# Optimization experiments

Measured on AMD Instinct MI355X. Metric: run time of the kernel, lower is better.

The kernel has to match this reference:

```python
import jax, jax.numpy as jnp
import numpy as np

N_NODES = 1601   # fixed by in_adj Parameter shape in the source
EMB = 300        # EMB_SIZE
LAYERS = 3       # process_num
B, L = 2048, 64  # batch_size, label_num


def setup_inputs() -> dict:
    key = jax.random.key(0)
    k1, k2, k3, k4 = jax.random.split(key, 4)
    return {
        "label_set": jax.random.randint(k1, (B, L), 0, N_NODES),
        "in_adj": jax.random.uniform(k2, (N_NODES, N_NODES), dtype=jnp.float32),
        "embeddings": jax.random.normal(k3, (N_NODES, EMB), dtype=jnp.float32),
        "linear_w": jax.random.normal(k4, (LAYERS, EMB, EMB), dtype=jnp.float32) * 0.05,
    }


def _norm_matrix(m):
    # m: [B, L, L]; add self loops, symmetric D^-1/2 A D^-1/2 with D = column sums
    n = m.shape[1]
    m = m + jnp.eye(n, dtype=m.dtype)
    d = jnp.sum(m, axis=1) ** -0.5            # [B, L] (sum over axis=1, as in torch code)
    return m * d[:, None, :] * d[:, :, None]


def reference(label_set, in_adj, embeddings, linear_w):
    # Gather per-batch dense neighbor adjacency: neighbor[b,i,j] = in_adj[label[b,i], label[b,j]]
    neighbor = in_adj[label_set[:, :, None], label_set[:, None, :]]   # [B, L, L]
    adj = _norm_matrix(neighbor)
    h = embeddings[label_set]                                          # [B, L, EMB]
    for i in range(linear_w.shape[0]):
        # linear projection (Linear bias=False: x @ W^T) then adjacency aggregation
        h = jnp.einsum('bij,bje->bie', adj, h @ linear_w[i].T)
    return h
```

## Files before the change

kernel.cpp:

```cpp
#include <hip/hip_runtime.h>

#define NN   1601
#define EMB  300
#define NB   2048
#define L    64
#define TSTR 304
#define S    72

typedef __attribute__((ext_vector_type(8))) short bf16x8;
typedef __attribute__((ext_vector_type(4))) float f32x4;

static __device__ __forceinline__ ushort f2b(float x) {
  union { float f; unsigned u; } c; c.f = x;
  unsigned u = c.u;
  return (ushort)((u + 0x7FFFu + ((u >> 16) & 1u)) >> 16);
}
static __device__ __forceinline__ float b2f(ushort h) {
  union { unsigned u; float f; } c; c.u = ((unsigned)h) << 16; return c.f;
}

#define LD8(p, r, c) (*(const bf16x8*)&(p)[(size_t)(r) * S + (c)])
#define MFMA(a, bm, acc) __builtin_amdgcn_mfma_f32_16x16x32_bf16((a), (bm), (acc), 0, 0, 0)

template <int BT, int BF16OUT>
__device__ __forceinline__ void gemm_body(ushort* arena,
                                          const float* __restrict__ A,
                                          const float* __restrict__ B,
                                          void* __restrict__ Cout,
                                          int M, int AS, int BS, int KG,
                                          int mb, int nb) {
  ushort* Ahi = arena;
  ushort* Alo = arena + L * S;
  ushort* Bhi = arena + 2 * L * S;
  ushort* Blo = arena + 3 * L * S;
  int tid = threadIdx.x;
  int lane = tid & 63, w = tid >> 6;
  int lrow = lane & 15, lk = lane >> 4;

  f32x4 acc[4];
  #pragma unroll
  for (int t = 0; t < 4; ++t) acc[t] = (f32x4){0.f, 0.f, 0.f, 0.f};

  for (int kc = 0; kc < 5; ++kc) {
    int k0 = 64 * kc;
    for (int idx = tid; idx < 64 * 16; idx += 256) {
      int r = idx >> 4, c4 = (idx & 15) * 4;
      int m = mb * 64 + r, k = k0 + c4;
      float4 v = make_float4(0.f, 0.f, 0.f, 0.f);
      if (m < M && k < KG) v = *(const float4*)&A[(size_t)m * AS + k];
      ushort4 h4, l4;
      h4.x = f2b(v.x); l4.x = f2b(v.x - b2f(h4.x));
      h4.y = f2b(v.y); l4.y = f2b(v.y - b2f(h4.y));
      h4.z = f2b(v.z); l4.z = f2b(v.z - b2f(h4.z));
      h4.w = f2b(v.w); l4.w = f2b(v.w - b2f(h4.w));
      *(ushort4*)&Ahi[r * S + c4] = h4;
      *(ushort4*)&Alo[r * S + c4] = l4;
    }
    for (int idx = tid; idx < 64 * 16; idx += 256) {
      int r = idx >> 4, c4 = (idx & 15) * 4;
      if (BT) {
        int n = nb * 64 + r, k = k0 + c4;
        float4 v = make_float4(0.f, 0.f, 0.f, 0.f);
        if (n < 300 && k < 300) v = *(const float4*)&B[(size_t)n * BS + k];
        ushort4 h4, l4;
        h4.x = f2b(v.x); l4.x = f2b(v.x - b2f(h4.x));
        h4.y = f2b(v.y); l4.y = f2b(v.y - b2f(h4.y));
        h4.z = f2b(v.z); l4.z = f2b(v.z - b2f(h4.z));
        h4.w = f2b(v.w); l4.w = f2b(v.w - b2f(h4.w));
        *(ushort4*)&Bhi[r * S + c4] = h4;
        *(ushort4*)&Blo[r * S + c4] = l4;
      } else {
        int k = k0 + r, n = nb * 64 + c4;
        float4 v = make_float4(0.f, 0.f, 0.f, 0.f);
        if (k < 300 && n < 300) v = *(const float4*)&B[(size_t)k * BS + n];
        #pragma unroll
        for (int q = 0; q < 4; ++q) {
          float xq = (q == 0) ? v.x : (q == 1) ? v.y : (q == 2) ? v.z : v.w;
          ushort hi = f2b(xq);
          Bhi[(size_t)(c4 + q) * S + r] = hi;
          Blo[(size_t)(c4 + q) * S + r] = f2b(xq - b2f(hi));
        }
      }
    }
    __syncthreads();
    #pragma unroll
    for (int ks = 0; ks < 2; ++ks) {
      bf16x8 ah = LD8(Ahi, 16 * w + lrow, 32 * ks + 8 * lk);
      bf16x8 al = LD8(Alo, 16 * w + lrow, 32 * ks + 8 * lk);
      #pragma unroll
      for (int t = 0; t < 4; ++t) {
        bf16x8 bh = LD8(Bhi, 16 * t + lrow, 32 * ks + 8 * lk);
        bf16x8 bl = LD8(Blo, 16 * t + lrow, 32 * ks + 8 * lk);
        acc[t] = MFMA(ah, bh, acc[t]);
        acc[t] = MFMA(ah, bl, acc[t]);
        acc[t] = MFMA(al, bh, acc[t]);
      }
    }
    __syncthreads();
  }
  #pragma unroll
  for (int t = 0; t < 4; ++t) {
    int n = nb * 64 + 16 * t + lrow;
    int mbase = mb * 64 + 16 * w + 4 * lk;
    if (n < TSTR) {
      #pragma unroll
      for (int r = 0; r < 4; ++r) {
        int m = mbase + r;
        if (m < M) {
          if (BF16OUT) ((ushort*)Cout)[(size_t)m * TSTR + n] = f2b(acc[t][r]);
          else         ((float*)Cout)[(size_t)m * TSTR + n] = acc[t][r];
        }
      }
    }
  }
}

__global__ __launch_bounds__(256, 4) void k_pre1(const float* __restrict__ in_adj,
                                                 unsigned char* __restrict__ adj8,
                                                 const float* __restrict__ emb,
                                                 const float* __restrict__ lw,
                                                 float* __restrict__ E1,
                                                 float* __restrict__ T) {
  __shared__ __align__(16) ushort arena[4 * L * S];
  const float* W1 = lw;
  const float* W2 = lw + (size_t)EMB * EMB;
  const float* W3 = lw + 2 * (size_t)EMB * EMB;
  int bid = blockIdx.x;
  if (bid < 25) {
    gemm_body<0, 0>(arena, W3, W2, T, 300, 300, 300, 300, bid / 5, bid % 5);
  } else if (bid < 155) {
    int rid = bid - 25;
    gemm_body<1, 0>(arena, emb, W1, E1, NN, 300, 300, 300, rid % 26, rid / 26);
  } else {
    int b2 = bid - 155;
    const int total = NN * NN;
    const int n4 = total >> 2;
    int i = b2 * 256 + threadIdx.x;
    for (int i4 = i; i4 < n4; i4 += 1024 * 256) {
      float4 v = *(const float4*)&in_adj[4 * i4];
      uchar4 q;
      q.x = (unsigned char)__float2int_rn(v.x * 255.f);
      q.y = (unsigned char)__float2int_rn(v.y * 255.f);
      q.z = (unsigned char)__float2int_rn(v.z * 255.f);
      q.w = (unsigned char)__float2int_rn(v.w * 255.f);
      *(uchar4*)&adj8[4 * i4] = q;
    }
    if (i == 0)
      adj8[total - 1] = (unsigned char)__float2int_rn(in_adj[total - 1] * 255.f);
  }
}

__device__ __forceinline__ void a3_body(ushort* arena, int* lab, float (*ps)[L],
                                        float* dv, const int* __restrict__ labels,
                                        const unsigned char* __restrict__ adj8,
                                        ushort* __restrict__ a3g, int b) {
  ushort* buf0 = arena;
  ushort* buf1 = arena + L * S;
  ushort* buf2 = arena + 2 * L * S;
  ushort* buf3 = arena + 3 * L * S;
  int tid = threadIdx.x, j = tid & 63, g = tid >> 6;
  if (tid < L) lab[tid] = labels[(size_t)b * L + tid];
  __syncthreads();
  int labj = lab[j];

  float raw[16];
  float cs = 0.f;
  #pragma unroll
  for (int q = 0; q < 16; ++q) {
    int i = g + 4 * q;
    float v = (float)adj8[(size_t)lab[i] * NN + labj];
    v += (i == j) ? 255.f : 0.f;
    raw[q] = v; cs += v;
  }
  ps[g][j] = cs;
  __syncthreads();
  if (tid < L) dv[tid] = 1.f / sqrtf(ps[0][tid] + ps[1][tid] + ps[2][tid] + ps[3][tid]);
  __syncthreads();

  float dj = dv[j];
  #pragma unroll
  for (int q = 0; q < 16; ++q) {
    int i = g + 4 * q;
    float a = raw[q] * dv[i] * dj;
    ushort hi = f2b(a);
    ushort lo = f2b(a - b2f(hi));
    buf0[(size_t)i * S + j] = hi;
    buf1[(size_t)i * S + j] = lo;
    buf2[(size_t)j * S + i] = hi;
    buf3[(size_t)j * S + i] = lo;
  }
  __syncthreads();

  int lane = tid & 63, w = tid >> 6;
  int lrow = lane & 15, lk = lane >> 4;
  int m0 = 16 * w;

  bf16x8 ah0 = LD8(buf0, m0 + lrow, 8 * lk);
  bf16x8 ah1 = LD8(buf0, m0 + lrow, 32 + 8 * lk);
  bf16x8 al0 = LD8(buf1, m0 + lrow, 8 * lk);
  bf16x8 al1 = LD8(buf1, m0 + lrow, 32 + 8 * lk);

  {
    f32x4 acc[4];
    #pragma unroll
    for (int t = 0; t < 4; ++t) {
      f32x4 a = {0.f, 0.f, 0.f, 0.f};
      bf16x8 bh = LD8(buf2, 16 * t + lrow, 8 * lk);
      bf16x8 bl = LD8(buf3, 16 * t + lrow, 8 * lk);
      a = MFMA(ah0, bh, a); a = MFMA(ah0, bl, a); a = MFMA(al0, bh, a);
      bh = LD8(buf2, 16 * t + lrow, 32 + 8 * lk);
      bl = LD8(buf3, 16 * t + lrow, 32 + 8 * lk);
      a = MFMA(ah1, bh, a); a = MFMA(ah1, bl, a); a = MFMA(al1, bh, a);
      acc[t] = a;
    }
    __syncthreads();
    #pragma unroll
    for (int t = 0; t < 4; ++t) {
      ushort4 h4, l4;
      float x;
      x = acc[t][0]; h4.x = f2b(x); l4.x = f2b(x - b2f(h4.x));
      x = acc[t][1]; h4.y = f2b(x); l4.y = f2b(x - b2f(h4.y));
      x = acc[t][2]; h4.z = f2b(x); l4.z = f2b(x - b2f(h4.z));
      x = acc[t][3]; h4.w = f2b(x); l4.w = f2b(x - b2f(h4.w));
      *(ushort4*)&buf2[(size_t)(16 * t + lrow) * S + m0 + 4 * lk] = h4;
      *(ushort4*)&buf3[(size_t)(16 * t + lrow) * S + m0 + 4 * lk] = l4;
    }
  }
  __syncthreads();

  {
    f32x4 acc[4];
    #pragma unroll
    for (int t = 0; t < 4; ++t) {
      f32x4 a = {0.f, 0.f, 0.f, 0.f};
      bf16x8 bh = LD8(buf2, 16 * t + lrow, 8 * lk);
      bf16x8 bl = LD8(buf3, 16 * t + lrow, 8 * lk);
      a = MFMA(ah0, bh, a); a = MFMA(ah0, bl, a); a = MFMA(al0, bh, a);
      bh = LD8(buf2, 16 * t + lrow, 32 + 8 * lk);
      bl = LD8(buf3, 16 * t + lrow, 32 + 8 * lk);
      a = MFMA(ah1, bh, a); a = MFMA(ah1, bl, a); a = MFMA(al1, bh, a);
      acc[t] = a;
    }
    #pragma unroll
    for (int t = 0; t < 4; ++t)
      #pragma unroll
      for (int r = 0; r < 4; ++r)
        buf0[(size_t)(m0 + 4 * lk + r) * S + 16 * t + lrow] = f2b(acc[t][r]);
  }
  __syncthreads();

  int4* dst = (int4*)(a3g + (size_t)b * (L * L));
  #pragma unroll
  for (int q = 0; q < 2; ++q) {
    int id = tid + 256 * q;
    int r = id >> 3, c8 = (id & 7) << 3;
    dst[id] = *(const int4*)&buf0[(size_t)r * S + c8];
  }
}

__global__ __launch_bounds__(256, 4) void k_pre2(const int* __restrict__ labels,
                                                 const unsigned char* __restrict__ adj8,
                                                 ushort* __restrict__ a3g,
                                                 const float* __restrict__ E1,
                                                 const float* __restrict__ T,
                                                 ushort* __restrict__ t0bf) {
  __shared__ __align__(16) ushort arena[4 * L * S];
  __shared__ int   lab[L];
  __shared__ float ps[4][L];
  __shared__ float dv[L];
  int bid = blockIdx.x;
  if (bid < NB) {
    a3_body(arena, lab, ps, dv, labels, adj8, a3g, bid);
  } else {
    int rid = bid - NB;
    gemm_body<1, 1>(arena, E1, T, t0bf, NN, TSTR, TSTR, TSTR, rid % 26, rid / 26);
  }
}

__global__ __launch_bounds__(256, 6) void k_out(const int* __restrict__ labels,
                                                const ushort* __restrict__ a3g,
                                                const ushort* __restrict__ t0bf,
                                                float* __restrict__ out) {
  __shared__ __align__(16) ushort A3L[L * S];
  __shared__ __align__(16) ushort Tt[80 * S];
  int bid = blockIdx.x;
  int b = bid >> 2, c = bid & 3;
  int tid = threadIdx.x, j = tid & 63, g = tid >> 6;
  int labj = labels[(size_t)b * L + j];

  const int4* a3p = (const int4*)(a3g + (size_t)b * (L * L));
  #pragma unroll
  for (int q = 0; q < 2; ++q) {
    int id = tid + 256 * q;
    int r = id >> 3, c8 = (id & 7) << 3;
    *(int4*)&A3L[(size_t)r * S + c8] = a3p[id];
  }
  int base = 80 * c;
  int rows80 = (c == 3) ? 64 : 80;
  const ushort* trow = t0bf + (size_t)labj * TSTR + base;
  for (int e = 8 * g; e < rows80; e += 32) {
    union { int4 v; ushort u[8]; } uu;
    uu.v = *(const int4*)(trow + e);
    #pragma unroll
    for (int q = 0; q < 8; ++q) Tt[(size_t)(e + q) * S + j] = uu.u[q];
  }
  __syncthreads();

  int lane = tid & 63, w = tid >> 6;
  int lrow = lane & 15, lk = lane >> 4;
  int m0 = 16 * w;
  bf16x8 fb0 = LD8(A3L, m0 + lrow, 8 * lk);
  bf16x8 fb1 = LD8(A3L, m0 + lrow, 32 + 8 * lk);
  float* orow = out + ((size_t)b * L + m0 + lrow) * EMB;

  int nt = (c == 3) ? 4 : 5;
  for (int t = 0; t < nt; ++t) {
    bf16x8 a0 = LD8(Tt, 16 * t + lrow, 8 * lk);
    bf16x8 a1 = LD8(Tt, 16 * t + lrow, 32 + 8 * lk);
    f32x4 o = {0.f, 0.f, 0.f, 0.f};
    o = MFMA(a0, fb0, o);
    o = MFMA(a1, fb1, o);
    int e0 = base + 16 * t + 4 * lk;
    if (e0 < EMB) *(f32x4*)&orow[e0] = o;
  }
}

extern "C" void kernel_launch(void* const* d_in, const int* in_sizes, int n_in,
                              void* d_out, int out_size, void* d_ws, size_t ws_size,
                              hipStream_t stream) {
  (void)in_sizes; (void)n_in; (void)out_size; (void)ws_size;
  const int*   labels = (const int*)d_in[0];
  const float* in_adj = (const float*)d_in[1];
  const float* emb    = (const float*)d_in[2];
  const float* lw     = (const float*)d_in[3];
  float* out = (float*)d_out;

  char* base = (char*)d_ws;
  unsigned char* adj8 = (unsigned char*)base;
  float*  T    = (float*)(base + 2563216);
  float*  E1   = (float*)(base + 2928016);
  ushort* t0bf = (ushort*)(base + 4874832);
  ushort* a3g  = (ushort*)(base + 5848240);

  k_pre1<<<1179, 256, 0, stream>>>(in_adj, adj8, emb, lw, E1, T);
  k_pre2<<<2178, 256, 0, stream>>>(labels, adj8, a3g, E1, T, t0bf);
  k_out <<<4 * NB, 256, 0, stream>>>(labels, a3g, t0bf, out);
}
```

Before: 108.9 us.

## Halve k_pre2 LDS arena to raise occupancy and reorder gemm blocks first

The adjacency-cube body now reuses two LDS buffers instead of four. It rebuilds the transposed hi/lo split after the A fragments are loaded into registers, which halves the shared-memory arena and lets the launch bound request 8 blocks per CU. A dedicated gemm2 body handles the E1·T product with the smaller arena, and its 130 blocks are scheduled ahead of the 2048 per-batch blocks so the long GEMM tiles start early. k_out's launch bound is raised to 7 and its output stores become nontemporal. The cost is extra barriers and a second pass of bf16 conversion writes.

```diff
diff --git a/kernel.cpp b/kernel.cpp
--- a/kernel.cpp
+++ b/kernel.cpp
@@ -110,6 +110,85 @@
           if (BF16OUT) ((ushort*)Cout)[(size_t)m * TSTR + n] = f2b(acc[t][r]);
           else         ((float*)Cout)[(size_t)m * TSTR + n] = acc[t][r];
         }
+      }
+    }
+  }
+}
+
+__device__ __forceinline__ void gemm2_body(ushort* arena,
+                                           const float* __restrict__ A,
+                                           const float* __restrict__ B,
+                                           ushort* __restrict__ Cout,
+                                           int M, int mb, int nb) {
+  ushort* buf0 = arena;
+  ushort* buf1 = arena + L * S;
+  int tid = threadIdx.x;
+  int lane = tid & 63, w = tid >> 6;
+  int lrow = lane & 15, lk = lane >> 4;
+
+  f32x4 acc[4];
+  #pragma unroll
+  for (int t = 0; t < 4; ++t) acc[t] = (f32x4){0.f, 0.f, 0.f, 0.f};
+
+  for (int kc = 0; kc < 5; ++kc) {
+    int k0 = 64 * kc;
+    for (int idx = tid; idx < 64 * 16; idx += 256) {
+      int r = idx >> 4, c4 = (idx & 15) * 4;
+      int m = mb * 64 + r, k = k0 + c4;
+      float4 v = make_float4(0.f, 0.f, 0.f, 0.f);
+      if (m < M && k < TSTR) v = *(const float4*)&A[(size_t)m * TSTR + k];
+      ushort4 h4, l4;
+      h4.x = f2b(v.x); l4.x = f2b(v.x - b2f(h4.x));
+      h4.y = f2b(v.y); l4.y = f2b(v.y - b2f(h4.y));
+      h4.z = f2b(v.z); l4.z = f2b(v.z - b2f(h4.z));
+      h4.w = f2b(v.w); l4.w = f2b(v.w - b2f(h4.w));
+      *(ushort4*)&buf0[r * S + c4] = h4;
+      *(ushort4*)&buf1[r * S + c4] = l4;
+    }
+    __syncthreads();
+    bf16x8 ah0 = LD8(buf0, 16 * w + lrow, 8 * lk);
+    bf16x8 ah1 = LD8(buf0, 16 * w + lrow, 32 + 8 * lk);
+    bf16x8 al0 = LD8(buf1, 16 * w + lrow, 8 * lk);
+    bf16x8 al1 = LD8(buf1, 16 * w + lrow, 32 + 8 * lk);
+    __syncthreads();
+    for (int idx = tid; idx < 64 * 16; idx += 256) {
+      int r = idx >> 4, c4 = (idx & 15) * 4;
+      int n = nb * 64 + r, k = k0 + c4;
+      float4 v = make_float4(0.f, 0.f, 0.f, 0.f);
+      if (n < 300 && k < TSTR) v = *(const float4*)&B[(size_t)n * TSTR + k];
+      ushort4 h4, l4;
+      h4.x = f2b(v.x); l4.x = f2b(v.x - b2f(h4.x));
+      h4.y = f2b(v.y); l4.y = f2b(v.y - b2f(h4.y));
+      h4.z = f2b(v.z); l4.z = f2b(v.z - b2f(h4.z));
+      h4.w = f2b(v.w); l4.w = f2b(v.w - b2f(h4.w));
+      *(ushort4*)&buf0[r * S + c4] = h4;
+      *(ushort4*)&buf1[r * S + c4] = l4;
+    }
+    __syncthreads();
+    #pragma unroll
+    for (int t = 0; t < 4; ++t) {
+      bf16x8 bh = LD8(buf0, 16 * t + lrow, 8 * lk);
+      bf16x8 bl = LD8(buf1, 16 * t + lrow, 8 * lk);
+      acc[t] = MFMA(ah0, bh, acc[t]);
+      acc[t] = MFMA(ah0, bl, acc[t]);
+      acc[t] = MFMA(al0, bh, acc[t]);
+      bh = LD8(buf0, 16 * t + lrow, 32 + 8 * lk);
+      bl = LD8(buf1, 16 * t + lrow, 32 + 8 * lk);
+      acc[t] = MFMA(ah1, bh, acc[t]);
+      acc[t] = MFMA(ah1, bl, acc[t]);
+      acc[t] = MFMA(al1, bh, acc[t]);
+    }
+    __syncthreads();
+  }
+  #pragma unroll
+  for (int t = 0; t < 4; ++t) {
+    int n = nb * 64 + 16 * t + lrow;
+    int mbase = mb * 64 + 16 * w + 4 * lk;
+    if (n < TSTR) {
+      #pragma unroll
+      for (int r = 0; r < 4; ++r) {
+        int m = mbase + r;
+        if (m < M) Cout[(size_t)m * TSTR + n] = f2b(acc[t][r]);
       }
     }
   }
@@ -156,8 +235,6 @@
                                         ushort* __restrict__ a3g, int b) {
   ushort* buf0 = arena;
   ushort* buf1 = arena + L * S;
-  ushort* buf2 = arena + 2 * L * S;
-  ushort* buf3 = arena + 3 * L * S;
   int tid = threadIdx.x, j = tid & 63, g = tid >> 6;
   if (tid < L) lab[tid] = labels[(size_t)b * L + tid];
   __syncthreads();
@@ -182,12 +259,10 @@
   for (int q = 0; q < 16; ++q) {
     int i = g + 4 * q;
     float a = raw[q] * dv[i] * dj;
+    raw[q] = a;
     ushort hi = f2b(a);
-    ushort lo = f2b(a - b2f(hi));
     buf0[(size_t)i * S + j] = hi;
-    buf1[(size_t)i * S + j] = lo;
-    buf2[(size_t)j * S + i] = hi;
-    buf3[(size_t)j * S + i] = lo;
+    buf1[(size_t)i * S + j] = f2b(a - b2f(hi));
   }
   __syncthreads();
 
@@ -199,17 +274,28 @@
   bf16x8 ah1 = LD8(buf0, m0 + lrow, 32 + 8 * lk);
   bf16x8 al0 = LD8(buf1, m0 + lrow, 8 * lk);
   bf16x8 al1 = LD8(buf1, m0 + lrow, 32 + 8 * lk);
+  __syncthreads();
+
+  #pragma unroll
+  for (int q = 0; q < 16; ++q) {
+    int i = g + 4 * q;
+    float a = raw[q];
+    ushort hi = f2b(a);
+    buf0[(size_t)j * S + i] = hi;
+    buf1[(size_t)j * S + i] = f2b(a - b2f(hi));
+  }
+  __syncthreads();
 
   {
     f32x4 acc[4];
     #pragma unroll
     for (int t = 0; t < 4; ++t) {
       f32x4 a = {0.f, 0.f, 0.f, 0.f};
-      bf16x8 bh = LD8(buf2, 16 * t + lrow, 8 * lk);
-      bf16x8 bl = LD8(buf3, 16 * t + lrow, 8 * lk);
+      bf16x8 bh = LD8(buf0, 16 * t + lrow, 8 * lk);
+      bf16x8 bl = LD8(buf1, 16 * t + lrow, 8 * lk);
       a = MFMA(ah0, bh, a); a = MFMA(ah0, bl, a); a = MFMA(al0, bh, a);
-      bh = LD8(buf2, 16 * t + lrow, 32 + 8 * lk);
-      bl = LD8(buf3, 16 * t + lrow, 32 + 8 * lk);
+      bh = LD8(buf0, 16 * t + lrow, 32 + 8 * lk);
+      bl = LD8(buf1, 16 * t + lrow, 32 + 8 * lk);
       a = MFMA(ah1, bh, a); a = MFMA(ah1, bl, a); a = MFMA(al1, bh, a);
       acc[t] = a;
     }
@@ -222,8 +308,8 @@
       x = acc[t][1]; h4.y = f2b(x); l4.y = f2b(x - b2f(h4.y));
       x = acc[t][2]; h4.z = f2b(x); l4.z = f2b(x - b2f(h4.z));
       x = acc[t][3]; h4.w = f2b(x); l4.w = f2b(x - b2f(h4.w));
-      *(ushort4*)&buf2[(size_t)(16 * t + lrow) * S + m0 + 4 * lk] = h4;
-      *(ushort4*)&buf3[(size_t)(16 * t + lrow) * S + m0 + 4 * lk] = l4;
+      *(ushort4*)&buf0[(size_t)(16 * t + lrow) * S + m0 + 4 * lk] = h4;
+      *(ushort4*)&buf1[(size_t)(16 * t + lrow) * S + m0 + 4 * lk] = l4;
     }
   }
   __syncthreads();
@@ -233,14 +319,15 @@
     #pragma unroll
     for (int t = 0; t < 4; ++t) {
       f32x4 a = {0.f, 0.f, 0.f, 0.f};
-      bf16x8 bh = LD8(buf2, 16 * t + lrow, 8 * lk);
-      bf16x8 bl = LD8(buf3, 16 * t + lrow, 8 * lk);
+      bf16x8 bh = LD8(buf0, 16 * t + lrow, 8 * lk);
+      bf16x8 bl = LD8(buf1, 16 * t + lrow, 8 * lk);
       a = MFMA(ah0, bh, a); a = MFMA(ah0, bl, a); a = MFMA(al0, bh, a);
-      bh = LD8(buf2, 16 * t + lrow, 32 + 8 * lk);
-      bl = LD8(buf3, 16 * t + lrow, 32 + 8 * lk);
+      bh = LD8(buf0, 16 * t + lrow, 32 + 8 * lk);
+      bl = LD8(buf1, 16 * t + lrow, 32 + 8 * lk);
       a = MFMA(ah1, bh, a); a = MFMA(ah1, bl, a); a = MFMA(al1, bh, a);
       acc[t] = a;
     }
+    __syncthreads();
     #pragma unroll
     for (int t = 0; t < 4; ++t)
       #pragma unroll
@@ -258,26 +345,25 @@
   }
 }
 
-__global__ __launch_bounds__(256, 4) void k_pre2(const int* __restrict__ labels,
+__global__ __launch_bounds__(256, 8) void k_pre2(const int* __restrict__ labels,
                                                  const unsigned char* __restrict__ adj8,
                                                  ushort* __restrict__ a3g,
                                                  const float* __restrict__ E1,
                                                  const float* __restrict__ T,
                                                  ushort* __restrict__ t0bf) {
-  __shared__ __align__(16) ushort arena[4 * L * S];
+  __shared__ __align__(16) ushort arena[2 * L * S];
   __shared__ int   lab[L];
   __shared__ float ps[4][L];
   __shared__ float dv[L];
   int bid = blockIdx.x;
-  if (bid < NB) {
-    a3_body(arena, lab, ps, dv, labels, adj8, a3g, bid);
+  if (bid < 130) {
+    gemm2_body(arena, E1, T, t0bf, NN, bid % 26, bid / 26);
   } else {
-    int rid = bid - NB;
-    gemm_body<1, 1>(arena, E1, T, t0bf, NN, TSTR, TSTR, TSTR, rid % 26, rid / 26);
-  }
-}
-
-__global__ __launch_bounds__(256, 6) void k_out(const int* __restrict__ labels,
+    a3_body(arena, lab, ps, dv, labels, adj8, a3g, bid - 130);
+  }
+}
+
+__global__ __launch_bounds__(256, 7) void k_out(const int* __restrict__ labels,
                                                 const ushort* __restrict__ a3g,
                                                 const ushort* __restrict__ t0bf,
                                                 float* __restrict__ out) {
@@ -321,7 +407,7 @@
     o = MFMA(a0, fb0, o);
     o = MFMA(a1, fb1, o);
     int e0 = base + 16 * t + 4 * lk;
-    if (e0 < EMB) *(f32x4*)&orow[e0] = o;
+    if (e0 < EMB) __builtin_nontemporal_store(o, (f32x4*)&orow[e0]);
   }
 }
 
```

New measurement: 173.0 us. +58.9%, slower.
